# Performance work log

Measured on AMD Instinct MI355X. Metric: run time of the kernel, lower is better.

## Reference

```python
import jax, jax.numpy as jnp
import numpy as np

B = 1
L_IMG, L_TMP, L_TXT = 1024, 1024, 256
D, H, HD, MLP = 1024, 16, 64, 4096
L = L_TXT + L_IMG + L_TMP
EPS = 1e-6
ATTN_SCALE = float(1.0 / np.sqrt(HD))


def setup_inputs() -> dict:
    key = jax.random.key(0)
    ks = jax.random.split(key, 12)
    s = 0.02  # keep activations stable
    return {
        'img': jax.random.normal(ks[0], (B, L_IMG, D), jnp.float32),
        'temporal': jax.random.normal(ks[1], (B, L_TMP, D), jnp.float32),
        'txt': jax.random.normal(ks[2], (B, L_TXT, D), jnp.float32),
        'vec': jax.random.normal(ks[3], (B, D), jnp.float32),
        'pe': jax.random.normal(ks[4], (B, 1, L, HD // 2, 2, 2), jnp.float32),
        'mod_w': jax.random.normal(ks[5], (3, D, 6 * D), jnp.float32) * s,
        'mod_b': jnp.zeros((3, 6 * D), jnp.float32),
        'qkv_w': jax.random.normal(ks[6], (3, D, 3 * D), jnp.float32) * s,
        'q_scale': jnp.ones((3, HD), jnp.float32),
        'k_scale': jnp.ones((3, HD), jnp.float32),
        'proj_w': jax.random.normal(ks[7], (3, D, D), jnp.float32) * s,
        'proj_b': jnp.zeros((3, D), jnp.float32),
        'mlp_w1': jax.random.normal(ks[8], (3, D, MLP), jnp.float32) * s,
        'mlp_b1': jnp.zeros((3, MLP), jnp.float32),
        'mlp_w2': jax.random.normal(ks[9], (3, MLP, D), jnp.float32) * s,
        'mlp_b2': jnp.zeros((3, D), jnp.float32),
    }


def _ln(x):
    # LayerNorm, elementwise_affine=False, eps=1e-6
    m = jnp.mean(x, axis=-1, keepdims=True)
    v = jnp.mean((x - m) ** 2, axis=-1, keepdims=True)
    return (x - m) * jax.lax.rsqrt(v + EPS)


def _rms(x, scale):
    # flux QKNorm RMSNorm with learnable per-head-dim scale
    return x * jax.lax.rsqrt(jnp.mean(x * x, axis=-1, keepdims=True) + EPS) * scale


def _rope(x, pe):
    # x: (B,H,L,HD), pe: (B,1,L,HD//2,2,2)
    xr = x.reshape(*x.shape[:-1], -1, 1, 2)
    out = pe[..., 0] * xr[..., 0] + pe[..., 1] * xr[..., 1]  # (B,H,L,HD//2,2)
    return out.reshape(x.shape)


def _forward(img, temporal, txt, vec, pe, mod_w, mod_b, qkv_w, q_scale, k_scale,
             proj_w, proj_b, mlp_w1, mlp_b1, mlp_w2, mlp_b2):
    sv = jax.nn.silu(vec)  # (B,D)

    def mods(i):
        m = (sv @ mod_w[i] + mod_b[i])[:, None, :]  # (B,1,6D)
        return jnp.split(m, 6, axis=-1)  # shift1, scale1, gate1, shift2, scale2, gate2

    def qkv_stream(x, i, shift1, scale1):
        xm = (1.0 + scale1) * _ln(x) + shift1
        qkv = (xm @ qkv_w[i]).reshape(x.shape[0], x.shape[1], 3, H, HD)
        q, k, v = jnp.moveaxis(qkv, 2, 0)  # each (B,Ls,H,HD)
        q = jnp.swapaxes(q, 1, 2)
        k = jnp.swapaxes(k, 1, 2)
        v = jnp.swapaxes(v, 1, 2)  # (B,H,Ls,HD)
        return _rms(q, q_scale[i]), _rms(k, k_scale[i]), v

    i_sh1, i_sc1, i_g1, i_sh2, i_sc2, i_g2 = mods(0)
    t_sh1, t_sc1, t_g1, t_sh2, t_sc2, t_g2 = mods(1)
    x_sh1, x_sc1, x_g1, x_sh2, x_sc2, x_g2 = mods(2)

    img_q, img_k, img_v = qkv_stream(img, 0, i_sh1, i_sc1)
    tmp_q, tmp_k, tmp_v = qkv_stream(temporal, 1, t_sh1, t_sc1)
    txt_q, txt_k, txt_v = qkv_stream(txt, 2, x_sh1, x_sc1)

    q = jnp.concatenate((txt_q, img_q, tmp_q), axis=2)
    k = jnp.concatenate((txt_k, img_k, tmp_k), axis=2)
    # NOTE: faithful to source bug: v concat uses temporal_q, not temporal_v
    v = jnp.concatenate((txt_v, img_v, tmp_q), axis=2)

    q = _rope(q, pe)
    k = _rope(k, pe)
    scores = jnp.einsum('bhqd,bhkd->bhqk', q, k) * ATTN_SCALE
    attn = jnp.einsum('bhqk,bhkd->bhqd', jax.nn.softmax(scores, axis=-1), v)
    attn = jnp.swapaxes(attn, 1, 2).reshape(attn.shape[0], L, H * HD)  # (B,L,D)

    txt_a = attn[:, :L_TXT]
    img_a = attn[:, L_TXT:L_TXT + L_IMG]
    tmp_a = attn[:, L_TXT + L_IMG:]

    def mlp(x, i):
        return jax.nn.gelu(x @ mlp_w1[i] + mlp_b1[i], approximate=True) @ mlp_w2[i] + mlp_b2[i]

    img = img + i_g1 * (img_a @ proj_w[0] + proj_b[0])
    img = img + i_g2 * mlp((1.0 + i_sc2) * _ln(img) + i_sh2, 0)
    temporal = temporal + t_g1 * (tmp_a @ proj_w[1] + proj_b[1])
    # NOTE: faithful to source bug: temporal_norm2 is applied to (updated) img
    temporal = temporal + t_g2 * mlp((1.0 + t_sc2) * _ln(img) + t_sh2, 1)
    txt = txt + x_g1 * (txt_a @ proj_w[2] + proj_b[2])
    txt = txt + x_g2 * mlp((1.0 + x_sc2) * _ln(txt) + x_sh2, 2)
    return img, temporal, txt


def reference(img, temporal, txt, vec, pe, mod_w, mod_b, qkv_w, q_scale, k_scale,
              proj_w, proj_b, mlp_w1, mlp_b1, mlp_w2, mlp_b2):
    return _forward(img, temporal, txt, vec, pe, mod_w, mod_b, qkv_w, q_scale,
                    k_scale, proj_w, proj_b, mlp_w1, mlp_b1, mlp_w2, mlp_b2)
```

## Files before the change

kernel.cpp:

```cpp
#include <hip/hip_runtime.h>
#include <hip/hip_bf16.h>

#define L_TXT 256
#define L_IMG 1024
#define L_TMP 1024
#define LTOT  2304
#define DMODEL 1024
#define NH 16
#define HDIM 64
#define DMLP 4096
#define EPSV 1e-6f

typedef unsigned short ushort;
typedef __attribute__((ext_vector_type(8))) short short8b;
typedef __attribute__((ext_vector_type(8))) unsigned short ushort8v;
typedef __attribute__((ext_vector_type(4))) float f32x4;
typedef __attribute__((ext_vector_type(4))) unsigned short ushort4v;

#define MOD_OFF    ((size_t)0)
#define XM_OFF     ((size_t)73728)
#define QKV_OFF    ((size_t)4792320)
#define QB_OFF     ((size_t)18948096)
#define KB_OFF     ((size_t)23666688)
#define VTB_OFF    ((size_t)28385280)
#define ATT_OFF    ((size_t)33103872)
#define S1_OFF     ((size_t)37822464)
#define QKVWT_OFF  ((size_t)49356800)
#define PROJWT_OFF ((size_t)68231168)
#define W1T_OFF    ((size_t)74522624)
#define W2T_OFF    ((size_t)99688448)
#define W2T_END    ((size_t)124854272)

static __device__ __forceinline__ ushort f2bf(float x) {
    __hip_bfloat16 b = __float2bfloat16(x);
    return *reinterpret_cast<ushort*>(&b);
}
static __device__ __forceinline__ float bf2f(ushort u) {
    return __uint_as_float(((unsigned)u) << 16);
}

typedef __attribute__((address_space(1))) const unsigned char gas_t;
typedef __attribute__((address_space(3))) unsigned char las_t;
static __device__ __forceinline__ void gload16(const void* g, void* l) {
    __builtin_amdgcn_global_load_lds((gas_t*)g, (las_t*)l, 16, 0, 0);
}

__global__ __launch_bounds__(256) void k_conv(const float* __restrict__ vec,
                                              const float* __restrict__ modw,
                                              float* __restrict__ modp,
                                              const float* __restrict__ qkvw,
                                              const float* __restrict__ projw,
                                              const float* __restrict__ w1,
                                              const float* __restrict__ w2,
                                              ushort* __restrict__ qkvwt,
                                              ushort* __restrict__ projwt,
                                              ushort* __restrict__ w1t,
                                              ushort* __restrict__ w2t) {
    __shared__ float tb[64][65];
    int bid = blockIdx.x;
    int tid = threadIdx.x;
    if (bid < 576) {
        float* svs = &tb[0][0];
        float* pl  = &tb[0][0] + 1024;
        int g0 = (bid >> 2) * 128;
        int ks = bid & 3;
        int i  = g0 / 6144;
        int j0 = g0 - i * 6144;
        {
            float v = vec[ks*256 + tid];
            svs[tid] = v / (1.0f + __expf(-v));
        }
        __syncthreads();
        int jl = tid & 31, ko = tid >> 5;
        const float* wp = modw + (size_t)i * 1024 * 6144 + (size_t)(ks*256) * 6144 + j0 + jl*4;
        float4 acc = {0.f,0.f,0.f,0.f};
#pragma unroll 8
        for (int kk = 0; kk < 32; kk++) {
            int k = kk*8 + ko;
            float4 wv = *reinterpret_cast<const float4*>(wp + (size_t)k * 6144);
            float s = svs[k];
            acc.x += s*wv.x; acc.y += s*wv.y; acc.z += s*wv.z; acc.w += s*wv.w;
        }
        pl[ko*128 + jl*4+0] = acc.x; pl[ko*128 + jl*4+1] = acc.y;
        pl[ko*128 + jl*4+2] = acc.z; pl[ko*128 + jl*4+3] = acc.w;
        __syncthreads();
        if (tid < 128) {
            float s = 0.f;
#pragma unroll
            for (int k = 0; k < 8; k++) s += pl[k*128 + tid];
            modp[(size_t)ks*18432 + g0 + tid] = s;
        }
        return;
    }
    int b = bid - 576;
    const float* W; ushort* WT; int K, N, nt, kt;
    if (b < 2304) {
        int s = b / 768, r = b % 768;
        K = 1024; N = 3072; nt = r % 48; kt = r / 48;
        W = qkvw + (size_t)s * K * N; WT = qkvwt + (size_t)s * N * K;
    } else if (b < 3072) {
        b -= 2304; int s = b / 256, r = b % 256;
        K = 1024; N = 1024; nt = r % 16; kt = r / 16;
        W = projw + (size_t)s * K * N; WT = projwt + (size_t)s * N * K;
    } else if (b < 6144) {
        b -= 3072; int s = b / 1024, r = b % 1024;
        K = 1024; N = 4096; nt = r % 64; kt = r / 64;
        W = w1 + (size_t)s * K * N; WT = w1t + (size_t)s * N * K;
    } else {
        b -= 6144; int s = b / 1024, r = b % 1024;
        K = 4096; N = 1024; nt = r % 16; kt = r / 16;
        W = w2 + (size_t)s * K * N; WT = w2t + (size_t)s * N * K;
    }
    {
        int r = tid >> 4, c4 = (tid & 15) * 4;
#pragma unroll
        for (int i = 0; i < 4; i++) {
            float4 v = *reinterpret_cast<const float4*>(W + (size_t)(kt*64 + r + i*16) * N + nt*64 + c4);
            tb[r + i*16][c4+0] = v.x; tb[r + i*16][c4+1] = v.y;
            tb[r + i*16][c4+2] = v.z; tb[r + i*16][c4+3] = v.w;
        }
    }
    __syncthreads();
    {
        int n  = tid >> 3;
        int k8 = (tid & 7) * 8;
#pragma unroll
        for (int half = 0; half < 2; half++) {
            int nn = n + half*32;
            ushort8v u;
#pragma unroll
            for (int i = 0; i < 8; i++) u[i] = f2bf(tb[k8+i][nn]);
            *reinterpret_cast<ushort8v*>(WT + (size_t)(nt*64 + nn) * K + kt*64 + k8) = u;
        }
    }
}

__global__ __launch_bounds__(256) void k_modr(const float* __restrict__ p,
                                              const float* __restrict__ modb,
                                              float* __restrict__ mod) {
    int g = blockIdx.x * 256 + threadIdx.x;
    float s = p[g] + p[18432 + g] + p[2*18432 + g] + p[3*18432 + g];
    mod[g] = s + modb[g];
}

__global__ __launch_bounds__(256) void k_conv_slice(const float* __restrict__ W,
                                                    ushort* __restrict__ WT,
                                                    int K, int N) {
    __shared__ float tb[64][65];
    int nt = blockIdx.x, kt = blockIdx.y, tid = threadIdx.x;
    {
        int r = tid >> 4, c4 = (tid & 15) * 4;
#pragma unroll
        for (int i = 0; i < 4; i++) {
            float4 v = *reinterpret_cast<const float4*>(W + (size_t)(kt*64 + r + i*16) * N + nt*64 + c4);
            tb[r + i*16][c4+0] = v.x; tb[r + i*16][c4+1] = v.y;
            tb[r + i*16][c4+2] = v.z; tb[r + i*16][c4+3] = v.w;
        }
    }
    __syncthreads();
    {
        int n  = tid >> 3;
        int k8 = (tid & 7) * 8;
#pragma unroll
        for (int half = 0; half < 2; half++) {
            int nn = n + half*32;
            ushort8v u;
#pragma unroll
            for (int i = 0; i < 8; i++) u[i] = f2bf(tb[k8+i][nn]);
            *reinterpret_cast<ushort8v*>(WT + (size_t)(nt*64 + nn) * K + kt*64 + k8) = u;
        }
    }
}

__global__ __launch_bounds__(256) void k_ln_mod1(const float* __restrict__ img,
                                                 const float* __restrict__ tmp,
                                                 const float* __restrict__ txt,
                                                 const float* __restrict__ mod,
                                                 ushort* __restrict__ xm) {
    int l = blockIdx.x;
    const float* src; int strm;
    if (l < L_TXT)              { src = txt + (size_t)l * DMODEL;            strm = 2; }
    else if (l < L_TXT + L_IMG) { src = img + (size_t)(l - L_TXT) * DMODEL;  strm = 0; }
    else                        { src = tmp + (size_t)(l - L_TXT - L_IMG) * DMODEL; strm = 1; }

    int d = threadIdx.x * 4;
    float4 x = *reinterpret_cast<const float4*>(src + d);
    float s  = x.x + x.y + x.z + x.w;
    float s2 = x.x*x.x + x.y*x.y + x.z*x.z + x.w*x.w;
#pragma unroll
    for (int o = 32; o > 0; o >>= 1) { s += __shfl_xor(s, o); s2 += __shfl_xor(s2, o); }
    __shared__ float red[8];
    int wave = threadIdx.x >> 6, lane = threadIdx.x & 63;
    if (lane == 0) { red[wave*2] = s; red[wave*2+1] = s2; }
    __syncthreads();
    if (threadIdx.x == 0) {
        float a = 0.f, b = 0.f;
        for (int w = 0; w < 4; w++) { a += red[w*2]; b += red[w*2+1]; }
        red[0] = a; red[1] = b;
    }
    __syncthreads();
    float mean = red[0] * (1.0f/DMODEL);
    float var  = red[1] * (1.0f/DMODEL) - mean*mean;
    float inv  = rsqrtf(var + EPSV);

    const float* sh = mod + strm*6144;
    const float* sc = sh + 1024;
    float4 shv = *reinterpret_cast<const float4*>(sh + d);
    float4 scv = *reinterpret_cast<const float4*>(sc + d);
    ushort4v o;
    o.x = f2bf((1.f+scv.x)*((x.x-mean)*inv) + shv.x);
    o.y = f2bf((1.f+scv.y)*((x.y-mean)*inv) + shv.y);
    o.z = f2bf((1.f+scv.z)*((x.z-mean)*inv) + shv.z);
    o.w = f2bf((1.f+scv.w)*((x.w-mean)*inv) + shv.w);
    *reinterpret_cast<ushort4v*>(xm + (size_t)l*DMODEL + d) = o;
}

__global__ __launch_bounds__(256) void k_ln_mod2(const float* __restrict__ src,
                                                 const float* __restrict__ sh,
                                                 const float* __restrict__ sc,
                                                 ushort* __restrict__ out) {
    int r = blockIdx.x;
    const float* srow = src + (size_t)r * DMODEL;
    int d = threadIdx.x * 4;
    float4 x = *reinterpret_cast<const float4*>(srow + d);
    float s  = x.x + x.y + x.z + x.w;
    float s2 = x.x*x.x + x.y*x.y + x.z*x.z + x.w*x.w;
#pragma unroll
    for (int o = 32; o > 0; o >>= 1) { s += __shfl_xor(s, o); s2 += __shfl_xor(s2, o); }
    __shared__ float red[8];
    int wave = threadIdx.x >> 6, lane = threadIdx.x & 63;
    if (lane == 0) { red[wave*2] = s; red[wave*2+1] = s2; }
    __syncthreads();
    if (threadIdx.x == 0) {
        float a = 0.f, b = 0.f;
        for (int w = 0; w < 4; w++) { a += red[w*2]; b += red[w*2+1]; }
        red[0] = a; red[1] = b;
    }
    __syncthreads();
    float mean = red[0] * (1.0f/DMODEL);
    float var  = red[1] * (1.0f/DMODEL) - mean*mean;
    float inv  = rsqrtf(var + EPSV);
    float4 shv = *reinterpret_cast<const float4*>(sh + d);
    float4 scv = *reinterpret_cast<const float4*>(sc + d);
    ushort4v o;
    o.x = f2bf((1.f+scv.x)*((x.x-mean)*inv) + shv.x);
    o.y = f2bf((1.f+scv.y)*((x.y-mean)*inv) + shv.y);
    o.z = f2bf((1.f+scv.z)*((x.z-mean)*inv) + shv.z);
    o.w = f2bf((1.f+scv.w)*((x.w-mean)*inv) + shv.w);
    *reinterpret_cast<ushort4v*>(out + (size_t)r*DMODEL + d) = o;
}

__global__ __launch_bounds__(256) void k_ln_modg(const float* __restrict__ s1,
                                                 const float* __restrict__ mod,
                                                 ushort* __restrict__ xm) {
    int row = blockIdx.x;
    int strm = row < 256 ? 2 : 0;
    const float* srow = s1 + (size_t)row * DMODEL;
    int d = threadIdx.x * 4;
    float4 x = *reinterpret_cast<const float4*>(srow + d);
    float s  = x.x + x.y + x.z + x.w;
    float s2 = x.x*x.x + x.y*x.y + x.z*x.z + x.w*x.w;
#pragma unroll
    for (int o = 32; o > 0; o >>= 1) { s += __shfl_xor(s, o); s2 += __shfl_xor(s2, o); }
    __shared__ float red[8];
    int wave = threadIdx.x >> 6, lane = threadIdx.x & 63;
    if (lane == 0) { red[wave*2] = s; red[wave*2+1] = s2; }
    __syncthreads();
    if (threadIdx.x == 0) {
        float a = 0.f, b = 0.f;
        for (int w = 0; w < 4; w++) { a += red[w*2]; b += red[w*2+1]; }
        red[0] = a; red[1] = b;
    }
    __syncthreads();
    float mean = red[0] * (1.0f/DMODEL);
    float var  = red[1] * (1.0f/DMODEL) - mean*mean;
    float inv  = rsqrtf(var + EPSV);
    const float* sh = mod + strm*6144 + 3*1024;
    const float* sc = mod + strm*6144 + 4*1024;
    float4 shv = *reinterpret_cast<const float4*>(sh + d);
    float4 scv = *reinterpret_cast<const float4*>(sc + d);
    ushort4v o;
    o.x = f2bf((1.f+scv.x)*((x.x-mean)*inv) + shv.x);
    o.y = f2bf((1.f+scv.y)*((x.y-mean)*inv) + shv.y);
    o.z = f2bf((1.f+scv.z)*((x.z-mean)*inv) + shv.z);
    o.w = f2bf((1.f+scv.w)*((x.w-mean)*inv) + shv.w);
    *reinterpret_cast<ushort4v*>(xm + (size_t)row*DMODEL + d) = o;
}

__device__ __forceinline__ float gelu_fast(float x) {
    return x / (1.0f + __expf(-1.5957691216057308f * (x + 0.044715f * x * x * x)));
}

template<int MODE, int BM, int BN, typename OutT>
__global__ __launch_bounds__(256) void k_gemm_ms(const ushort* __restrict__ A_t,
                                                 const ushort* __restrict__ A_i,
                                                 const ushort* __restrict__ A_m,
                                                 const ushort* __restrict__ BT,
                                                 const float* __restrict__ bias,
                                                 const float* __restrict__ res_t,
                                                 const float* __restrict__ res_i,
                                                 const float* __restrict__ res_m,
                                                 const float* __restrict__ mod, int gidx,
                                                 OutT* __restrict__ out_t,
                                                 OutT* __restrict__ out_i,
                                                 OutT* __restrict__ out_m,
                                                 int N, int K, int ry0) {
    constexpr int MI = BM / 32;
    constexpr int NI = BN / 32;
    const int brow = (ry0 + blockIdx.y) * BM;
    int s, lrow;
    if (brow < 256)       { s = 2; lrow = brow; }
    else if (brow < 1280) { s = 0; lrow = brow - 256; }
    else                  { s = 1; lrow = brow - 1280; }

    const ushort* A = (s==2 ? A_t : s==0 ? A_i : A_m) + (size_t)lrow * K;
    const ushort* BTs = BT + (size_t)s * N * K;
    const float* bi = bias ? bias + (size_t)s * N : nullptr;
    const float* resl = (MODE==2) ? ((s==2 ? res_t : s==0 ? res_i : res_m) + (size_t)lrow * N) : nullptr;
    const float* gate = (MODE==2) ? (mod + s*6144 + gidx*1024) : nullptr;
    OutT* Cl = (s==2 ? out_t : s==0 ? out_i : out_m) + (size_t)lrow * N;

    __shared__ ushort Asl[BM*64];
    __shared__ ushort Bsl[BN*64];
    const int tid = threadIdx.x;
    const int lane = tid & 63, w = tid >> 6;
    const int wr = w >> 1, wc = w & 1;
    const int bn = blockIdx.x * BN;
    const int r15 = lane & 15, g4 = lane >> 4;

    f32x4 acc[MI][NI];
#pragma unroll
    for (int i = 0; i < MI; i++)
#pragma unroll
        for (int j = 0; j < NI; j++) acc[i][j] = (f32x4){0.f,0.f,0.f,0.f};

    for (int k0 = 0; k0 < K; k0 += 64) {
#pragma unroll
        for (int i = 0; i < BM/32; i++) {
            int chunk = i*4 + w;
            int seg = chunk*64 + lane;
            int row = seg >> 3;
            int gs  = (seg & 7) ^ (row & 7);
            gload16(A + (size_t)row * K + k0 + gs*8, Asl + (size_t)chunk * 512);
        }
#pragma unroll
        for (int i = 0; i < BN/32; i++) {
            int chunk = i*4 + w;
            int seg = chunk*64 + lane;
            int row = seg >> 3;
            int gs  = (seg & 7) ^ (row & 7);
            gload16(BTs + (size_t)(bn + row) * K + k0 + gs*8, Bsl + (size_t)chunk * 512);
        }
        __syncthreads();
#pragma unroll
        for (int kk = 0; kk < 2; kk++) {
            short8b a[MI], b[NI];
#pragma unroll
            for (int mi = 0; mi < MI; mi++) {
                int row = wr*(MI*16) + mi*16 + r15;
                int c   = kk*4 + g4;
                a[mi] = *reinterpret_cast<const short8b*>(&Asl[row*64 + ((c ^ (row & 7)))*8]);
            }
#pragma unroll
            for (int ni = 0; ni < NI; ni++) {
                int row = wc*(NI*16) + ni*16 + r15;
                int c   = kk*4 + g4;
                b[ni] = *reinterpret_cast<const short8b*>(&Bsl[row*64 + ((c ^ (row & 7)))*8]);
            }
#pragma unroll
            for (int mi = 0; mi < MI; mi++)
#pragma unroll
                for (int ni = 0; ni < NI; ni++)
                    acc[mi][ni] = __builtin_amdgcn_mfma_f32_16x16x32_bf16(a[mi], b[ni], acc[mi][ni], 0, 0, 0);
        }
        __syncthreads();
    }

#pragma unroll
    for (int mi = 0; mi < MI; mi++) {
#pragma unroll
        for (int ni = 0; ni < NI; ni++) {
            int col = bn + wc*(NI*16) + ni*16 + r15;
            float bv = bi ? bi[col] : 0.f;
#pragma unroll
            for (int r = 0; r < 4; r++) {
                int rr = wr*(MI*16) + mi*16 + g4*4 + r;
                float v = acc[mi][ni][r] + bv;
                if (MODE == 1) v = gelu_fast(v);
                if (MODE == 2) v = resl[(size_t)rr * N + col] + gate[col] * v;
                if (sizeof(OutT) == 2) Cl[(size_t)rr * N + col] = (OutT)f2bf(v);
                else                   Cl[(size_t)rr * N + col] = (OutT)v;
            }
        }
    }
}

__global__ __launch_bounds__(256) void k_qkvfin(const ushort* __restrict__ qkv,
                                                const float* __restrict__ pe,
                                                const float* __restrict__ qs,
                                                const float* __restrict__ ks,
                                                ushort* __restrict__ Q,
                                                ushort* __restrict__ K,
                                                ushort* __restrict__ VT) {
    const int tid = threadIdx.x;
    const int w = tid >> 6, lane = tid & 63;
    const int h  = blockIdx.x / 36;
    const int l0 = (blockIdx.x % 36) * 64;
    __shared__ ushort vbuf[64][65];

    for (int it = 0; it < 16; it++) {
        int ll = it*4 + w;
        int l = l0 + ll;
        int strm;
        if (l < L_TXT) strm = 2; else if (l < L_TXT + L_IMG) strm = 0; else strm = 1;
        const ushort* row = qkv + (size_t)l * 3 * DMODEL + h*HDIM + lane;
        float q = bf2f(row[0]);
        float k = bf2f(row[DMODEL]);
        float v = bf2f(row[2*DMODEL]);

        float sq = q*q, sk = k*k;
#pragma unroll
        for (int o = 32; o > 0; o >>= 1) { sq += __shfl_xor(sq, o); sk += __shfl_xor(sk, o); }
        float rq = q * rsqrtf(sq * (1.0f/HDIM) + EPSV) * qs[strm*HDIM + lane];
        float rk = k * rsqrtf(sk * (1.0f/HDIM) + EPSV) * ks[strm*HDIM + lane];

        float vout = (strm == 1) ? rq : v;

        float rq_p = __shfl_xor(rq, 1);
        float rk_p = __shfl_xor(rk, 1);
        float qe = (lane & 1) ? rq_p : rq;
        float qo = (lane & 1) ? rq : rq_p;
        float ke = (lane & 1) ? rk_p : rk;
        float ko = (lane & 1) ? rk : rk_p;
        const float* pel = pe + (size_t)l*128 + (lane >> 1)*4 + (lane & 1)*2;
        float qr = pel[0]*qe + pel[1]*qo;
        float kr = pel[0]*ke + pel[1]*ko;

        size_t idx = ((size_t)h * LTOT + l) * HDIM + lane;
        Q[idx] = f2bf(qr);
        K[idx] = f2bf(kr);
        vbuf[ll][lane] = f2bf(vout);
    }
    __syncthreads();
    {
        int d = tid >> 2, ls = (tid & 3) * 16;
        ushort8v u0, u1;
#pragma unroll
        for (int i = 0; i < 8; i++) u0[i] = vbuf[ls+i][d];
#pragma unroll
        for (int i = 0; i < 8; i++) u1[i] = vbuf[ls+8+i][d];
        ushort* dst = VT + ((size_t)h * 64 + d) * LTOT + l0 + ls;
        *reinterpret_cast<ushort8v*>(dst)     = u0;
        *reinterpret_cast<ushort8v*>(dst + 8) = u1;
    }
}

__global__ __launch_bounds__(256) void k_attn_mfma(const ushort* __restrict__ Qb,
                                                   const ushort* __restrict__ Kb,
                                                   const ushort* __restrict__ VTb,
                                                   ushort* __restrict__ att) {
    const int tid = threadIdx.x;
    const int w = tid >> 6, lane = tid & 63;
    const int h  = blockIdx.x / 36;
    const int qt = blockIdx.x % 36;
    const int qbase = qt*64 + w*16;
    const int g = lane >> 4;
    const int q = lane & 15;

    __shared__ ushort Ksl[2][64*64];
    __shared__ ushort Vsl[2][64*64];
    __shared__ ushort plds[4][1024];
    ushort* P = plds[w];

    const ushort* Kg = Kb  + (size_t)h * LTOT * 64;
    const ushort* Vg = VTb + (size_t)h * 64 * LTOT;

    const ushort* qp = Qb + ((size_t)h * LTOT + qbase + q) * 64 + g*8;
    const short8b qf0 = *reinterpret_cast<const short8b*>(qp);
    const short8b qf1 = *reinterpret_cast<const short8b*>(qp + 32);

    f32x4 out[4];
#pragma unroll
    for (int d = 0; d < 4; d++) out[d] = (f32x4){0.f,0.f,0.f,0.f};
    float m = -1e30f, lsum = 0.f;

#pragma unroll
    for (int i = 0; i < 2; i++) {
        int seg = i*256 + tid;
        int row = seg >> 3;
        int gs  = (seg & 7) ^ (row & 7);
        gload16(Kg + (size_t)row*64 + gs*8, &Ksl[0][(size_t)(i*256 + w*64)*8]);
        gload16(Vg + (size_t)row*LTOT + gs*8, &Vsl[0][(size_t)(i*256 + w*64)*8]);
    }

    for (int t = 0; t < 36; t++) {
        const int cb = t & 1;
        __syncthreads();
        if (t < 35) {
            int kvn = (t+1) * 64;
#pragma unroll
            for (int i = 0; i < 2; i++) {
                int seg = i*256 + tid;
                int row = seg >> 3;
                int gs  = (seg & 7) ^ (row & 7);
                gload16(Kg + (size_t)(kvn + row)*64 + gs*8, &Ksl[cb^1][(size_t)(i*256 + w*64)*8]);
                gload16(Vg + (size_t)row*LTOT + kvn + gs*8, &Vsl[cb^1][(size_t)(i*256 + w*64)*8]);
            }
        }

        f32x4 s[4];
        __builtin_amdgcn_s_setprio(1);
#pragma unroll
        for (int ks = 0; ks < 4; ks++) {
            int r = ks*16 + q;
            short8b kf0 = *reinterpret_cast<const short8b*>(&Ksl[cb][r*64 + ((g     ^ (r & 7)))*8]);
            short8b kf1 = *reinterpret_cast<const short8b*>(&Ksl[cb][r*64 + (((4+g) ^ (r & 7)))*8]);
            f32x4 acc = (f32x4){0.f,0.f,0.f,0.f};
            acc = __builtin_amdgcn_mfma_f32_16x16x32_bf16(kf0, qf0, acc, 0, 0, 0);
            acc = __builtin_amdgcn_mfma_f32_16x16x32_bf16(kf1, qf1, acc, 0, 0, 0);
            s[ks] = acc;
        }
        __builtin_amdgcn_s_setprio(0);
        float tmax = -1e30f;
#pragma unroll
        for (int ks = 0; ks < 4; ks++)
#pragma unroll
            for (int r = 0; r < 4; r++) tmax = fmaxf(tmax, s[ks][r]);
        tmax = fmaxf(tmax, __shfl_xor(tmax, 16));
        tmax = fmaxf(tmax, __shfl_xor(tmax, 32));
        float newm = fmaxf(m, tmax * 0.125f);
        float c = __expf(m - newm);
        float p[16];
        float tsum = 0.f;
#pragma unroll
        for (int ks = 0; ks < 4; ks++)
#pragma unroll
            for (int r = 0; r < 4; r++) {
                float pv = __expf(s[ks][r] * 0.125f - newm);
                p[ks*4+r] = pv;
                tsum += pv;
            }
        tsum += __shfl_xor(tsum, 16);
        tsum += __shfl_xor(tsum, 32);
        lsum = lsum * c + tsum;
        m = newm;
#pragma unroll
        for (int d = 0; d < 4; d++) out[d] *= c;

#pragma unroll
        for (int ks = 0; ks < 4; ks++) {
            ushort4v pk;
            pk.x = f2bf(p[ks*4+0]); pk.y = f2bf(p[ks*4+1]);
            pk.z = f2bf(p[ks*4+2]); pk.w = f2bf(p[ks*4+3]);
            int widx = (q*64 + ks*16 + g*4) ^ ((q & 7) << 3);
            *reinterpret_cast<ushort4v*>(&P[widx]) = pk;
        }
        __builtin_amdgcn_s_setprio(1);
#pragma unroll
        for (int c2 = 0; c2 < 2; c2++) {
            int ridx = (q*64 + c2*32 + g*8) ^ ((q & 7) << 3);
            short8b pf = *reinterpret_cast<const short8b*>(&P[ridx]);
#pragma unroll
            for (int ds = 0; ds < 4; ds++) {
                int d = ds*16 + q;
                short8b vf = *reinterpret_cast<const short8b*>(&Vsl[cb][d*64 + (((c2*4+g) ^ (d & 7)))*8]);
                out[ds] = __builtin_amdgcn_mfma_f32_16x16x32_bf16(vf, pf, out[ds], 0, 0, 0);
            }
        }
        __builtin_amdgcn_s_setprio(0);
    }

    float inv = 1.0f / lsum;
    ushort* orow = att + (size_t)(qbase + q) * DMODEL + h * HDIM;
#pragma unroll
    for (int ds = 0; ds < 4; ds++) {
        ushort4v o4;
        o4.x = f2bf(out[ds][0]*inv); o4.y = f2bf(out[ds][1]*inv);
        o4.z = f2bf(out[ds][2]*inv); o4.w = f2bf(out[ds][3]*inv);
        *reinterpret_cast<ushort4v*>(orow + ds*16 + g*4) = o4;
    }
}

extern "C" void kernel_launch(void* const* d_in, const int* in_sizes, int n_in,
                              void* d_out, int out_size, void* d_ws, size_t ws_size,
                              hipStream_t stream) {
    const float* img  = (const float*)d_in[0];
    const float* tmp  = (const float*)d_in[1];
    const float* txt  = (const float*)d_in[2];
    const float* vec  = (const float*)d_in[3];
    const float* pe   = (const float*)d_in[4];
    const float* modw = (const float*)d_in[5];
    const float* modb = (const float*)d_in[6];
    const float* qkvw = (const float*)d_in[7];
    const float* qsc  = (const float*)d_in[8];
    const float* ksc  = (const float*)d_in[9];
    const float* projw= (const float*)d_in[10];
    const float* projb= (const float*)d_in[11];
    const float* w1   = (const float*)d_in[12];
    const float* b1   = (const float*)d_in[13];
    const float* w2   = (const float*)d_in[14];
    const float* b2   = (const float*)d_in[15];

    char* wsb = (char*)d_ws;
    float*  mod    = (float*) (wsb + MOD_OFF);
    ushort* xm     = (ushort*)(wsb + XM_OFF);
    ushort* qkv    = (ushort*)(wsb + QKV_OFF);
    ushort* t1     = (ushort*)(wsb + QKV_OFF);
    ushort* Qb     = (ushort*)(wsb + QB_OFF);
    ushort* Kb     = (ushort*)(wsb + KB_OFF);
    ushort* VTb    = (ushort*)(wsb + VTB_OFF);
    float*  modp   = (float*) (wsb + ATT_OFF);
    ushort* att    = (ushort*)(wsb + ATT_OFF);
    float*  s1     = (float*) (wsb + S1_OFF);
    ushort* qkvwt  = (ushort*)(wsb + QKVWT_OFF);
    ushort* projwt = (ushort*)(wsb + PROJWT_OFF);
    ushort* w1t    = (ushort*)(wsb + W1T_OFF);

    const bool bigws = ws_size >= W2T_END;
    ushort* w2t = bigws ? (ushort*)(wsb + W2T_OFF) : w1t;

    float* out_img = (float*)d_out;
    float* out_tmp = out_img + (size_t)L_IMG * DMODEL;
    float* out_txt = out_tmp + (size_t)L_TMP * DMODEL;

    int conv_blocks = 576 + (bigws ? 9216 : 6144);
    k_conv<<<conv_blocks, 256, 0, stream>>>(vec, modw, modp,
                                            qkvw, projw, w1, w2,
                                            qkvwt, projwt, w1t, w2t);
    k_modr<<<72, 256, 0, stream>>>(modp, modb, mod);
    k_ln_mod1<<<LTOT, 256, 0, stream>>>(img, tmp, txt, mod, xm);

    k_gemm_ms<0, 128, 128, ushort><<<dim3(24, 18), 256, 0, stream>>>(
        xm, xm + (size_t)256*DMODEL, xm + (size_t)1280*DMODEL,
        qkvwt, nullptr, nullptr, nullptr, nullptr, nullptr, 0,
        qkv, qkv + (size_t)256*3072, qkv + (size_t)1280*3072, 3072, DMODEL, 0);

    k_qkvfin<<<NH*36, 256, 0, stream>>>(qkv, pe, qsc, ksc, Qb, Kb, VTb);
    k_attn_mfma<<<NH*36, 256, 0, stream>>>(Qb, Kb, VTb, att);

    k_gemm_ms<2, 64, 128, float><<<dim3(8, 36), 256, 0, stream>>>(
        att, att + (size_t)256*DMODEL, att + (size_t)1280*DMODEL,
        projwt, projb, txt, img, tmp, mod, 2,
        s1, s1 + (size_t)256*DMODEL, s1 + (size_t)1280*DMODEL, DMODEL, DMODEL, 0);

    k_ln_modg<<<1280, 256, 0, stream>>>(s1, mod, xm);
    k_gemm_ms<1, 128, 128, ushort><<<dim3(32, 10), 256, 0, stream>>>(
        xm, xm + (size_t)256*DMODEL, xm + (size_t)1280*DMODEL,
        w1t, b1, nullptr, nullptr, nullptr, nullptr, 0,
        t1, t1 + (size_t)256*DMLP, t1, DMLP, DMODEL, 0);
    if (!bigws) {
        k_conv_slice<<<dim3(16, 64), 256, 0, stream>>>(w2,                          w1t,                          DMLP, DMODEL);
        k_conv_slice<<<dim3(16, 64), 256, 0, stream>>>(w2 + (size_t)2*DMLP*DMODEL,  w1t + (size_t)2*DMLP*DMODEL,  DMLP, DMODEL);
    }
    k_gemm_ms<2, 64, 64, float><<<dim3(16, 20), 256, 0, stream>>>(
        t1, t1 + (size_t)256*DMLP, t1,
        w2t, b2, s1, s1 + (size_t)256*DMODEL, s1 + (size_t)1280*DMODEL, mod, 5,
        out_txt, out_img, out_tmp, DMODEL, DMLP, 0);

    k_ln_mod2<<<L_TMP, 256, 0, stream>>>(out_img, mod + 1*6144 + 3*1024, mod + 1*6144 + 4*1024, xm + (size_t)1280*DMODEL);
    k_gemm_ms<1, 128, 128, ushort><<<dim3(32, 8), 256, 0, stream>>>(
        xm, xm + (size_t)256*DMODEL, xm + (size_t)1280*DMODEL,
        w1t, b1, nullptr, nullptr, nullptr, nullptr, 0,
        t1, t1, t1, DMLP, DMODEL, 10);
    if (!bigws) {
        k_conv_slice<<<dim3(16, 64), 256, 0, stream>>>(w2 + (size_t)DMLP*DMODEL, w1t + (size_t)DMLP*DMODEL, DMLP, DMODEL);
    }
    k_gemm_ms<2, 64, 64, float><<<dim3(16, 16), 256, 0, stream>>>(
        t1, t1, t1,
        w2t, b2, s1, s1, s1 + (size_t)1280*DMODEL, mod, 5,
        out_txt, out_img, out_tmp, DMODEL, DMLP, 20);
}
```

Measured before the change: 327.8 us.

## Widen weight-transpose tiles, split mod-GEMV accumulators, skip redundant softmax rescale

The weight-conversion kernels now transpose 64x128 tiles instead of 64x64, with each thread writing four contiguous 16-byte chunks, which halves the block count and should make the bf16 stores more contiguous. The modulation GEMV uses two independent accumulator sets to expose more memory-level parallelism. In attention, the online-softmax max uses a tree reduction, and the rescale of the running sum and output is skipped when no lane's max grows. The larger LDS tile (64x132 floats) may lower occupancy, and the 132-float row stride can cause bank conflicts when reading columns during the transpose.

```diff
diff --git a/kernel.cpp b/kernel.cpp
--- a/kernel.cpp
+++ b/kernel.cpp
@@ -56,12 +56,12 @@
                                               ushort* __restrict__ projwt,
                                               ushort* __restrict__ w1t,
                                               ushort* __restrict__ w2t) {
-    __shared__ float tb[64][65];
+    __shared__ float tb[64][132];
     int bid = blockIdx.x;
     int tid = threadIdx.x;
     if (bid < 576) {
         float* svs = &tb[0][0];
-        float* pl  = &tb[0][0] + 1024;
+        float* pl  = &tb[0][0] + 256;
         int g0 = (bid >> 2) * 128;
         int ks = bid & 3;
         int i  = g0 / 6144;
@@ -73,16 +73,22 @@
         __syncthreads();
         int jl = tid & 31, ko = tid >> 5;
         const float* wp = modw + (size_t)i * 1024 * 6144 + (size_t)(ks*256) * 6144 + j0 + jl*4;
-        float4 acc = {0.f,0.f,0.f,0.f};
-#pragma unroll 8
-        for (int kk = 0; kk < 32; kk++) {
-            int k = kk*8 + ko;
-            float4 wv = *reinterpret_cast<const float4*>(wp + (size_t)k * 6144);
-            float s = svs[k];
-            acc.x += s*wv.x; acc.y += s*wv.y; acc.z += s*wv.z; acc.w += s*wv.w;
-        }
-        pl[ko*128 + jl*4+0] = acc.x; pl[ko*128 + jl*4+1] = acc.y;
-        pl[ko*128 + jl*4+2] = acc.z; pl[ko*128 + jl*4+3] = acc.w;
+        float a0x=0.f,a0y=0.f,a0z=0.f,a0w=0.f;
+        float a1x=0.f,a1y=0.f,a1z=0.f,a1w=0.f;
+#pragma unroll 4
+        for (int kk = 0; kk < 16; kk++) {
+            int k0 = kk*16 + ko;
+            int k1 = k0 + 8;
+            float4 w0 = *reinterpret_cast<const float4*>(wp + (size_t)k0 * 6144);
+            float4 w1v = *reinterpret_cast<const float4*>(wp + (size_t)k1 * 6144);
+            float s0 = svs[k0], s1 = svs[k1];
+            a0x += s0*w0.x; a0y += s0*w0.y; a0z += s0*w0.z; a0w += s0*w0.w;
+            a1x += s1*w1v.x; a1y += s1*w1v.y; a1z += s1*w1v.z; a1w += s1*w1v.w;
+        }
+        pl[ko*128 + jl*4+0] = a0x + a1x;
+        pl[ko*128 + jl*4+1] = a0y + a1y;
+        pl[ko*128 + jl*4+2] = a0z + a1z;
+        pl[ko*128 + jl*4+3] = a0w + a1w;
         __syncthreads();
         if (tid < 128) {
             float s = 0.f;
@@ -94,43 +100,42 @@
     }
     int b = bid - 576;
     const float* W; ushort* WT; int K, N, nt, kt;
-    if (b < 2304) {
-        int s = b / 768, r = b % 768;
-        K = 1024; N = 3072; nt = r % 48; kt = r / 48;
+    if (b < 1152) {
+        int s = b / 384, r = b % 384;
+        K = 1024; N = 3072; nt = r % 24; kt = r / 24;
         W = qkvw + (size_t)s * K * N; WT = qkvwt + (size_t)s * N * K;
+    } else if (b < 1536) {
+        b -= 1152; int s = b / 128, r = b % 128;
+        K = 1024; N = 1024; nt = r % 8; kt = r / 8;
+        W = projw + (size_t)s * K * N; WT = projwt + (size_t)s * N * K;
     } else if (b < 3072) {
-        b -= 2304; int s = b / 256, r = b % 256;
-        K = 1024; N = 1024; nt = r % 16; kt = r / 16;
-        W = projw + (size_t)s * K * N; WT = projwt + (size_t)s * N * K;
-    } else if (b < 6144) {
-        b -= 3072; int s = b / 1024, r = b % 1024;
-        K = 1024; N = 4096; nt = r % 64; kt = r / 64;
+        b -= 1536; int s = b / 512, r = b % 512;
+        K = 1024; N = 4096; nt = r % 32; kt = r / 32;
         W = w1 + (size_t)s * K * N; WT = w1t + (size_t)s * N * K;
     } else {
-        b -= 6144; int s = b / 1024, r = b % 1024;
-        K = 4096; N = 1024; nt = r % 16; kt = r / 16;
+        b -= 3072; int s = b / 512, r = b % 512;
+        K = 4096; N = 1024; nt = r % 8; kt = r / 8;
         W = w2 + (size_t)s * K * N; WT = w2t + (size_t)s * N * K;
     }
     {
-        int r = tid >> 4, c4 = (tid & 15) * 4;
-#pragma unroll
-        for (int i = 0; i < 4; i++) {
-            float4 v = *reinterpret_cast<const float4*>(W + (size_t)(kt*64 + r + i*16) * N + nt*64 + c4);
-            tb[r + i*16][c4+0] = v.x; tb[r + i*16][c4+1] = v.y;
-            tb[r + i*16][c4+2] = v.z; tb[r + i*16][c4+3] = v.w;
+        int r = tid >> 5, c4 = (tid & 31) * 4;
+#pragma unroll
+        for (int i = 0; i < 8; i++) {
+            float4 v = *reinterpret_cast<const float4*>(W + (size_t)(kt*64 + r + i*8) * N + nt*128 + c4);
+            tb[r + i*8][c4+0] = v.x; tb[r + i*8][c4+1] = v.y;
+            tb[r + i*8][c4+2] = v.z; tb[r + i*8][c4+3] = v.w;
         }
     }
     __syncthreads();
     {
-        int n  = tid >> 3;
-        int k8 = (tid & 7) * 8;
-#pragma unroll
-        for (int half = 0; half < 2; half++) {
-            int nn = n + half*32;
+        int n = tid >> 1, k32 = (tid & 1) * 32;
+        ushort* dst = WT + (size_t)(nt*128 + n) * K + kt*64 + k32;
+#pragma unroll
+        for (int j2 = 0; j2 < 4; j2++) {
             ushort8v u;
 #pragma unroll
-            for (int i = 0; i < 8; i++) u[i] = f2bf(tb[k8+i][nn]);
-            *reinterpret_cast<ushort8v*>(WT + (size_t)(nt*64 + nn) * K + kt*64 + k8) = u;
+            for (int i = 0; i < 8; i++) u[i] = f2bf(tb[k32 + j2*8 + i][n]);
+            *reinterpret_cast<ushort8v*>(dst + j2*8) = u;
         }
     }
 }
@@ -146,28 +151,27 @@
 __global__ __launch_bounds__(256) void k_conv_slice(const float* __restrict__ W,
                                                     ushort* __restrict__ WT,
                                                     int K, int N) {
-    __shared__ float tb[64][65];
+    __shared__ float tb[64][132];
     int nt = blockIdx.x, kt = blockIdx.y, tid = threadIdx.x;
     {
-        int r = tid >> 4, c4 = (tid & 15) * 4;
-#pragma unroll
-        for (int i = 0; i < 4; i++) {
-            float4 v = *reinterpret_cast<const float4*>(W + (size_t)(kt*64 + r + i*16) * N + nt*64 + c4);
-            tb[r + i*16][c4+0] = v.x; tb[r + i*16][c4+1] = v.y;
-            tb[r + i*16][c4+2] = v.z; tb[r + i*16][c4+3] = v.w;
+        int r = tid >> 5, c4 = (tid & 31) * 4;
+#pragma unroll
+        for (int i = 0; i < 8; i++) {
+            float4 v = *reinterpret_cast<const float4*>(W + (size_t)(kt*64 + r + i*8) * N + nt*128 + c4);
+            tb[r + i*8][c4+0] = v.x; tb[r + i*8][c4+1] = v.y;
+            tb[r + i*8][c4+2] = v.z; tb[r + i*8][c4+3] = v.w;
         }
     }
     __syncthreads();
     {
-        int n  = tid >> 3;
-        int k8 = (tid & 7) * 8;
-#pragma unroll
-        for (int half = 0; half < 2; half++) {
-            int nn = n + half*32;
+        int n = tid >> 1, k32 = (tid & 1) * 32;
+        ushort* dst = WT + (size_t)(nt*128 + n) * K + kt*64 + k32;
+#pragma unroll
+        for (int j2 = 0; j2 < 4; j2++) {
             ushort8v u;
 #pragma unroll
-            for (int i = 0; i < 8; i++) u[i] = f2bf(tb[k8+i][nn]);
-            *reinterpret_cast<ushort8v*>(WT + (size_t)(nt*64 + nn) * K + kt*64 + k8) = u;
+            for (int i = 0; i < 8; i++) u[i] = f2bf(tb[k32 + j2*8 + i][n]);
+            *reinterpret_cast<ushort8v*>(dst + j2*8) = u;
         }
     }
 }
@@ -521,31 +525,39 @@
             s[ks] = acc;
         }
         __builtin_amdgcn_s_setprio(0);
-        float tmax = -1e30f;
-#pragma unroll
-        for (int ks = 0; ks < 4; ks++)
-#pragma unroll
-            for (int r = 0; r < 4; r++) tmax = fmaxf(tmax, s[ks][r]);
+
+        float m0 = fmaxf(fmaxf(s[0][0], s[0][1]), s[0][2]);
+        float m1 = fmaxf(fmaxf(s[0][3], s[1][0]), s[1][1]);
+        float m2 = fmaxf(fmaxf(s[1][2], s[1][3]), s[2][0]);
+        float m3 = fmaxf(fmaxf(s[2][1], s[2][2]), s[2][3]);
+        float m4 = fmaxf(fmaxf(s[3][0], s[3][1]), s[3][2]);
+        float t5 = fmaxf(fmaxf(m0, m1), m2);
+        float t6 = fmaxf(fmaxf(m3, m4), s[3][3]);
+        float tmax = fmaxf(t5, t6);
         tmax = fmaxf(tmax, __shfl_xor(tmax, 16));
         tmax = fmaxf(tmax, __shfl_xor(tmax, 32));
-        float newm = fmaxf(m, tmax * 0.125f);
-        float c = __expf(m - newm);
+        float pm = tmax * 0.125f;
+        if (!__all(pm <= m)) {
+            float newm = fmaxf(m, pm);
+            float c = __expf(m - newm);
+            lsum *= c;
+#pragma unroll
+            for (int d = 0; d < 4; d++) out[d] *= c;
+            m = newm;
+        }
         float p[16];
         float tsum = 0.f;
 #pragma unroll
         for (int ks = 0; ks < 4; ks++)
 #pragma unroll
             for (int r = 0; r < 4; r++) {
-                float pv = __expf(s[ks][r] * 0.125f - newm);
+                float pv = __expf(s[ks][r] * 0.125f - m);
                 p[ks*4+r] = pv;
                 tsum += pv;
             }
         tsum += __shfl_xor(tsum, 16);
         tsum += __shfl_xor(tsum, 32);
-        lsum = lsum * c + tsum;
-        m = newm;
-#pragma unroll
-        for (int d = 0; d < 4; d++) out[d] *= c;
+        lsum += tsum;
 
 #pragma unroll
         for (int ks = 0; ks < 4; ks++) {
@@ -623,7 +635,7 @@
     float* out_tmp = out_img + (size_t)L_IMG * DMODEL;
     float* out_txt = out_tmp + (size_t)L_TMP * DMODEL;
 
-    int conv_blocks = 576 + (bigws ? 9216 : 6144);
+    int conv_blocks = 576 + (bigws ? 4608 : 3072);
     k_conv<<<conv_blocks, 256, 0, stream>>>(vec, modw, modp,
                                             qkvw, projw, w1, w2,
                                             qkvwt, projwt, w1t, w2t);
@@ -649,8 +661,8 @@
         w1t, b1, nullptr, nullptr, nullptr, nullptr, 0,
         t1, t1 + (size_t)256*DMLP, t1, DMLP, DMODEL, 0);
     if (!bigws) {
-        k_conv_slice<<<dim3(16, 64), 256, 0, stream>>>(w2,                          w1t,                          DMLP, DMODEL);
-        k_conv_slice<<<dim3(16, 64), 256, 0, stream>>>(w2 + (size_t)2*DMLP*DMODEL,  w1t + (size_t)2*DMLP*DMODEL,  DMLP, DMODEL);
+        k_conv_slice<<<dim3(8, 64), 256, 0, stream>>>(w2,                          w1t,                          DMLP, DMODEL);
+        k_conv_slice<<<dim3(8, 64), 256, 0, stream>>>(w2 + (size_t)2*DMLP*DMODEL,  w1t + (size_t)2*DMLP*DMODEL,  DMLP, DMODEL);
     }
     k_gemm_ms<2, 64, 64, float><<<dim3(16, 20), 256, 0, stream>>>(
         t1, t1 + (size_t)256*DMLP, t1,
@@ -663,7 +675,7 @@
         w1t, b1, nullptr, nullptr, nullptr, nullptr, 0,
         t1, t1, t1, DMLP, DMODEL, 10);
     if (!bigws) {
-        k_conv_slice<<<dim3(16, 64), 256, 0, stream>>>(w2 + (size_t)DMLP*DMODEL, w1t + (size_t)DMLP*DMODEL, DMLP, DMODEL);
+        k_conv_slice<<<dim3(8, 64), 256, 0, stream>>>(w2 + (size_t)DMLP*DMODEL, w1t + (size_t)DMLP*DMODEL, DMLP, DMODEL);
     }
     k_gemm_ms<2, 64, 64, float><<<dim3(16, 16), 256, 0, stream>>>(
         t1, t1, t1,
```

Result: no change. 328.8 us (+0.3%).
